# Performance work log

Measured on AMD Instinct MI355X. Metric: run time of the kernel, lower is better.

Reference implementation:

```python
import jax, jax.numpy as jnp
import numpy as np

SUB_NO = 20
T_NO = 200
T_DATA = 200000
E_NO = 400
I_NO = 100
N_BASIS = 20
COS_SHIFT = 1.0
COS_SCALE = 5.0


def make_cos_basis():
    # (N_BASIS, T_NO) raised-cosine basis in log time
    i = jnp.arange(N_BASIS, dtype=jnp.float32)[:, None]
    phi = (jnp.pi / 2.0) * i
    x = jnp.arange(T_NO, dtype=jnp.float32)[None, :]
    raw = COS_SCALE * jnp.log(x + COS_SHIFT)
    basis = 0.5 * jnp.cos(raw - phi) + 0.5
    keep = (raw >= phi - jnp.pi) & (raw <= phi + jnp.pi)
    return jnp.where(keep, basis, 0.0)


def grouped_causal_conv(syn, kern_flipped):
    # syn: (T, sub), kern_flipped: (sub, T_NO) already time-reversed -> causal filter
    x = jnp.pad(syn.T, ((0, 0), (T_NO - 1, 0)))[None]          # (1, sub, T+T_NO-1)
    out = jax.lax.conv_general_dilated(
        x, kern_flipped[:, None, :], (1,), 'VALID',
        dimension_numbers=('NCH', 'OIH', 'NCH'),
        feature_group_count=syn.shape[1])
    return out[0].T                                             # (T, sub)


def causal_conv1(z_pad, kern_flipped):
    # z_pad: (L,), kern_flipped: (T_NO,) -> valid conv, length L - T_NO + 1
    out = jax.lax.conv_general_dilated(
        z_pad[None, None, :], kern_flipped[None, None, :], (1,), 'VALID',
        dimension_numbers=('NCH', 'OIH', 'NCH'))
    return out[0, 0]


def setup_inputs() -> dict:
    key = jax.random.key(0)
    ks = jax.random.split(key, 12)
    S_e = (jax.random.uniform(ks[0], (T_DATA, E_NO)) < 0.05).astype(jnp.float32)
    S_i = (jax.random.uniform(ks[1], (T_DATA, I_NO)) < 0.05).astype(jnp.float32)
    Z = (jax.random.uniform(ks[2], (T_DATA,)) < 0.02).astype(jnp.float32)
    # binary-tree dendrite adjacency
    C_den = np.zeros((SUB_NO, SUB_NO), dtype=np.int32)
    for c in range(1, SUB_NO):
        C_den[(c - 1) // 2, c] = 1
    C_den = jnp.asarray(C_den)
    e_asn = np.asarray(jax.random.randint(ks[3], (E_NO,), 0, SUB_NO))
    i_asn = np.asarray(jax.random.randint(ks[4], (I_NO,), 0, SUB_NO))
    C_syn_e = np.zeros((SUB_NO, E_NO), dtype=np.float32); C_syn_e[e_asn, np.arange(E_NO)] = 1.0
    C_syn_i = np.zeros((SUB_NO, I_NO), dtype=np.float32); C_syn_i[i_asn, np.arange(I_NO)] = 1.0
    W_syn_ns = jax.random.uniform(ks[5], (SUB_NO, 2)) * 0.1
    W_syn_ns = W_syn_ns.at[:, 1].multiply(-1.0)
    return {
        'S_e': S_e, 'S_i': S_i, 'Z': Z,
        'C_den': C_den,
        'C_syn_e': jnp.asarray(C_syn_e), 'C_syn_i': jnp.asarray(C_syn_i),
        'W_syn_ns': W_syn_ns,
        'Tau_syn_ns': jnp.ones((SUB_NO, 2)) * 3.0,
        'Delta_syn_ns': jnp.zeros((SUB_NO, 2)),
        'W_syn_s': jax.random.normal(ks[6], (SUB_NO, N_BASIS, 2)) * 0.01,
        'W_sub_ns': jnp.ones(SUB_NO) * 0.1,
        'W_sub_s': jnp.ones(SUB_NO) * 0.1,
        'V_o': jax.random.normal(ks[7], (1,)),
        'Theta_ns': jnp.zeros(SUB_NO),
        'Theta_s': jnp.zeros(SUB_NO),
        'hist_s_weights': jax.random.normal(ks[8], (N_BASIS,)) * 0.01,
        'hist_ns_weights': jax.random.normal(ks[9], (N_BASIS,)) * 0.01,
    }


def reference(S_e, S_i, Z, C_den, C_syn_e, C_syn_i, W_syn_ns, Tau_syn_ns,
              Delta_syn_ns, W_syn_s, W_sub_ns, W_sub_s, V_o, Theta_ns,
              Theta_s, hist_s_weights, hist_ns_weights):
    cos_basis = make_cos_basis()
    # --- spike_convolve ---
    syn_e = S_e @ C_syn_e.T                                     # (T, sub)
    syn_i = S_i @ C_syn_i.T
    t = jnp.arange(T_NO, dtype=jnp.float32)[None, :]
    tau_e = Tau_syn_ns[:, 0:1] ** 2
    tau_i = Tau_syn_ns[:, 1:2] ** 2
    t_e = jnp.maximum(t - Delta_syn_ns[:, 0:1], 0.0) / tau_e
    t_i = jnp.maximum(t - Delta_syn_ns[:, 1:2], 0.0) / tau_i
    e_kern_ns = t_e * jnp.exp(-t_e) * W_syn_ns[:, 0:1] ** 2      # (sub, T_NO)
    i_kern_ns = -t_i * jnp.exp(-t_i) * W_syn_ns[:, 1:2] ** 2
    e_kern_s = (W_syn_s[:, :, 0] ** 2) @ cos_basis               # (sub, T_NO)
    i_kern_s = -(W_syn_s[:, :, 1] ** 2) @ cos_basis
    filt_e_ns = grouped_causal_conv(syn_e, jnp.flip(e_kern_ns, 1))
    filt_i_ns = grouped_causal_conv(syn_i, jnp.flip(i_kern_ns, 1))
    filt_e_s = grouped_causal_conv(syn_e, jnp.flip(e_kern_s, 1))
    filt_i_s = grouped_causal_conv(syn_i, jnp.flip(i_kern_s, 1))
    syn_ns = filt_e_ns + filt_i_ns
    syn_s = filt_e_s + filt_i_s
    # --- spike-history filtering of observed root spikes Z ---
    hist_s_kern = hist_s_weights @ cos_basis                     # (T_NO,)
    hist_ns_kern = hist_ns_weights @ cos_basis
    Z_pad = jnp.pad(Z, (T_NO, 0))                                # (T + T_NO,)
    hist_ns_filt = causal_conv1(Z_pad, jnp.flip(hist_ns_kern))[:-1]  # (T,)
    hist_s_filt = causal_conv1(Z_pad, jnp.flip(hist_s_kern))[:-1]
    # --- leaf-to-root tree recursion (unrolled over SUB_NO static nodes) ---
    C_den_f = C_den.astype(syn_s.dtype)
    w_s2 = W_sub_s ** 2
    w_ns2 = W_sub_ns ** 2
    T_data = S_e.shape[0]
    s_out = jnp.zeros((T_data, SUB_NO), dtype=syn_s.dtype)
    ns_out = jnp.zeros((T_data, SUB_NO), dtype=syn_ns.dtype)
    for idx in range(SUB_NO - 1, 0, -1):
        child_s = s_out @ (C_den_f[idx] * w_s2)                  # (T,) 0 if leaf
        child_ns = ns_out @ (C_den_f[idx] * w_ns2)
        s_out = s_out.at[:, idx].set(jnp.tanh(syn_s[:, idx] + child_s + Theta_s[idx]))
        ns_out = ns_out.at[:, idx].set(jnp.tanh(syn_ns[:, idx] + child_ns + Theta_ns[idx]))
    root_child_s = s_out @ (C_den_f[0] * w_s2)
    root_child_ns = ns_out @ (C_den_f[0] * w_ns2)
    s0 = jax.nn.sigmoid(hist_s_filt + syn_s[:, 0] + root_child_s + Theta_s[0])
    ns0 = jnp.tanh(hist_ns_filt + syn_ns[:, 0] + root_child_ns + Theta_ns[0])
    final_V = ns0 * w_ns2[0] + V_o
    final_Z = s0
    out_filters = jnp.vstack((e_kern_ns, i_kern_ns, e_kern_s, i_kern_s,
                              hist_ns_kern[None, :], hist_s_kern[None, :]))
    return final_V, final_Z, out_filters
```

## Files before the change

### kernel.cpp

```cpp
#include <hip/hip_runtime.h>

#define T_DATA 200000
#define E_NO 400
#define I_NO 100
#define SUB_NO 20
#define N_BASIS 20
#define T_NO 200

typedef unsigned short u16;
typedef unsigned int u32;
typedef unsigned long long u64;

#define WS_K4    0
#define WS_HIST2 64000
#define WS_MASKS 65600
#define WS_SYNE  131072
#define WS_SYNI  (WS_SYNE + 8000000)
#define WS_SNS   (WS_SYNI + 8000000)
#define WS_SS    (WS_SNS + 8000000)
#define WS_HF    (WS_SS + 8000000)

__device__ __forceinline__ u16 f2bf(float f) {
    union { float f; u32 u; } v; v.f = f;
    u32 u = v.u;
    u32 lsb = (u >> 16) & 1u;
    u += 0x7fffu + lsb;
    return (u16)(u >> 16);
}
__device__ __forceinline__ float bf2f(u16 b) {
    union { u32 u; float f; } v; v.u = ((u32)b) << 16; return v.f;
}
__device__ __forceinline__ void unpack8(uint4 u, float* x) {
    union { u32 u; float f; } c;
    c.u = u.x << 16;          x[0] = c.f;
    c.u = u.x & 0xffff0000u;  x[1] = c.f;
    c.u = u.y << 16;          x[2] = c.f;
    c.u = u.y & 0xffff0000u;  x[3] = c.f;
    c.u = u.z << 16;          x[4] = c.f;
    c.u = u.z & 0xffff0000u;  x[5] = c.f;
    c.u = u.w << 16;          x[6] = c.f;
    c.u = u.w & 0xffff0000u;  x[7] = c.f;
}
__device__ __forceinline__ float fast_tanh(float x) {
    x = fminf(fmaxf(x, -15.f), 15.f);
    float e = __expf(2.f * x);
    return 1.f - 2.f / (e + 1.f);
}
__device__ __forceinline__ float fast_sigmoid(float x) {
    x = fminf(fmaxf(x, -30.f), 30.f);
    return 1.f / (1.f + __expf(-x));
}

__global__ __launch_bounds__(256) void k_setup(
    const float* __restrict__ Wns, const float* __restrict__ Tau,
    const float* __restrict__ Del, const float* __restrict__ Wsyns,
    const float* __restrict__ HwS, const float* __restrict__ HwNS,
    const float* __restrict__ Cse, const float* __restrict__ Csi,
    float4* __restrict__ k4, float2* __restrict__ hist2,
    u32* __restrict__ masks32, float* __restrict__ outF)
{
    __shared__ float cb[N_BASIS * T_NO];
    __shared__ u32 m32[480];
    const int tid = threadIdx.x;
    const int b = blockIdx.x;
    const float PI = 3.14159265358979323846f;

    if (b == 21) {
        for (int k = tid; k < 480; k += 256) m32[k] = 0;
        __syncthreads();
        for (int j = tid; j < E_NO; j += 256) {
            int a = 0;
            for (int s = 0; s < SUB_NO; ++s)
                if (Cse[s * E_NO + j] > 0.5f) a = s;
            int ch = j >> 8, r = j & 255, ln = r >> 2, cp = r & 3;
            int widx = (a * 8 + ch * 4 + cp) * 2 + (ln >> 5);
            atomicOr(&m32[widx], 1u << (ln & 31));
        }
        for (int j = tid; j < I_NO; j += 256) {
            int a = 0;
            for (int s = 0; s < SUB_NO; ++s)
                if (Csi[s * I_NO + j] > 0.5f) a = s;
            int ln = j >> 2, cp = j & 3;
            int widx = 320 + (a * 4 + cp) * 2 + (ln >> 5);
            atomicOr(&m32[widx], 1u << (ln & 31));
        }
        __syncthreads();
        for (int k = tid; k < 480; k += 256) masks32[k] = m32[k];
        return;
    }

    for (int it = tid; it < N_BASIS * T_NO; it += 256) {
        int bb = it / T_NO, j = it - bb * T_NO;
        float phi = 1.57079632679489662f * (float)bb;
        float raw = 5.0f * logf((float)j + 1.0f);
        float v = 0.f;
        if (raw >= phi - PI && raw <= phi + PI) v = 0.5f * cosf(raw - phi) + 0.5f;
        cb[it] = v;
    }
    __syncthreads();

    if (b < 20) {
        const int s = b;
        if (tid < T_NO) {
            const int j = tid;
            float tau_e = Tau[s * 2 + 0]; tau_e *= tau_e;
            float tau_i = Tau[s * 2 + 1]; tau_i *= tau_i;
            float de = Del[s * 2 + 0], di = Del[s * 2 + 1];
            float we = Wns[s * 2 + 0]; we *= we;
            float wi = Wns[s * 2 + 1]; wi *= wi;
            float te = fmaxf((float)j - de, 0.f) / tau_e;
            float ti = fmaxf((float)j - di, 0.f) / tau_i;
            float eNs = te * expf(-te) * we;
            float iNs = -ti * expf(-ti) * wi;
            float eS = 0.f, iS = 0.f;
            for (int bb = 0; bb < N_BASIS; ++bb) {
                float w0 = Wsyns[(s * N_BASIS + bb) * 2 + 0];
                float w1 = Wsyns[(s * N_BASIS + bb) * 2 + 1];
                float c = cb[bb * T_NO + j];
                eS += w0 * w0 * c;
                iS -= w1 * w1 * c;
            }
            int it = s * T_NO + j;
            k4[it] = make_float4(eNs, iNs, eS, iS);
            outF[it]         = eNs;
            outF[4000 + it]  = iNs;
            outF[8000 + it]  = eS;
            outF[12000 + it] = iS;
        }
    } else {
        if (tid < T_NO) {
            const int j = tid;
            float hn = 0.f, hs = 0.f;
            for (int bb = 0; bb < N_BASIS; ++bb) {
                float c = cb[bb * T_NO + j];
                hn += HwNS[bb] * c;
                hs += HwS[bb] * c;
            }
            hist2[j] = make_float2(hn, hs);
            outF[16000 + j] = hn;
            outF[16200 + j] = hs;
        }
    }
}

__global__ __launch_bounds__(256) void k_spikes(
    const float* __restrict__ Se, const float* __restrict__ Si,
    const u64* __restrict__ masks,
    u16* __restrict__ synEb, u16* __restrict__ synIb)
{
    __shared__ u16 tile[4][40 * 66];
    const int tid = threadIdx.x;
    const int wv = tid >> 6, lane = tid & 63;
    const int t0 = (blockIdx.x * 4 + wv) * 64;
    if (t0 >= T_DATA) return;

    u64 me0 = 0, me1 = 0, me2 = 0, me3 = 0, me4 = 0, me5 = 0, me6 = 0, me7 = 0;
    u64 mi0 = 0, mi1 = 0, mi2 = 0, mi3 = 0;
    if (lane < 20) {
        const u64* mp = masks + lane * 8;
        me0 = mp[0]; me1 = mp[1]; me2 = mp[2]; me3 = mp[3];
        me4 = mp[4]; me5 = mp[5]; me6 = mp[6]; me7 = mp[7];
    } else if (lane < 40) {
        const u64* mp = masks + 160 + (lane - 20) * 4;
        mi0 = mp[0]; mi1 = mp[1]; mi2 = mp[2]; mi3 = mp[3];
    }
    u16* tw = tile[wv];

#pragma unroll 2
    for (int tt = 0; tt < 64; ++tt) {
        const int t = t0 + tt;
        const float4* rE = (const float4*)(Se + (size_t)t * E_NO);
        const float4* rI = (const float4*)(Si + (size_t)t * I_NO);
        float4 e0 = rE[lane];
        float4 e1 = make_float4(0.f, 0.f, 0.f, 0.f);
        if (lane < 36) e1 = rE[64 + lane];
        float4 i0 = make_float4(0.f, 0.f, 0.f, 0.f);
        if (lane < 25) i0 = rI[lane];
        u64 b0 = __ballot(e0.x != 0.f);
        u64 b1 = __ballot(e0.y != 0.f);
        u64 b2 = __ballot(e0.z != 0.f);
        u64 b3 = __ballot(e0.w != 0.f);
        u64 b4 = __ballot(e1.x != 0.f);
        u64 b5 = __ballot(e1.y != 0.f);
        u64 b6 = __ballot(e1.z != 0.f);
        u64 b7 = __ballot(e1.w != 0.f);
        u64 c0 = __ballot(i0.x != 0.f);
        u64 c1 = __ballot(i0.y != 0.f);
        u64 c2 = __ballot(i0.z != 0.f);
        u64 c3 = __ballot(i0.w != 0.f);
        if (lane < 20) {
            int c = __popcll(b0 & me0) + __popcll(b1 & me1)
                  + __popcll(b2 & me2) + __popcll(b3 & me3)
                  + __popcll(b4 & me4) + __popcll(b5 & me5)
                  + __popcll(b6 & me6) + __popcll(b7 & me7);
            tw[lane * 66 + tt] = (u16)c;
        } else if (lane < 40) {
            int c = __popcll(c0 & mi0) + __popcll(c1 & mi1)
                  + __popcll(c2 & mi2) + __popcll(c3 & mi3);
            tw[lane * 66 + tt] = (u16)c;
        }
    }
    asm volatile("s_waitcnt lgkmcnt(0)" ::: "memory");

#pragma unroll 4
    for (int s = 0; s < 40; ++s) {
        float f = (float)tw[s * 66 + lane];
        u16 b = f2bf(f);
        if (s < 20) synEb[(size_t)s * T_DATA + t0 + lane] = b;
        else        synIb[(size_t)(s - 20) * T_DATA + t0 + lane] = b;
    }
}

#define TT 512
#define WROW 712
__global__ __launch_bounds__(256) void k_conv(
    const u16* __restrict__ synEb, const u16* __restrict__ synIb,
    const float* __restrict__ Z,
    const float4* __restrict__ k4g, const float2* __restrict__ hist2g,
    u16* __restrict__ synNSb, u16* __restrict__ synSb,
    float2* __restrict__ hfilt)
{
    __shared__ __align__(16) u16 wE[4 * WROW];
    __shared__ __align__(16) u16 wI[4 * WROW];
    __shared__ __align__(16) float4 k4l[4 * T_NO];
    const int tid = threadIdx.x;
    const int t0 = blockIdx.x * TT;
    const int g  = blockIdx.y;
    const int W0 = t0 - 200;

    if (g < 5) {
        for (int q = tid; q < 712; q += 256) {
            int arr = (q >= 356) ? 1 : 0;
            int qq = q - arr * 356;
            int row = qq / 89, c = qq - row * 89;
            int s = g * 4 + row;
            const u16* src = (arr ? synIb : synEb) + (size_t)s * T_DATA;
            u16* dst = (arr ? wI : wE) + row * WROW + c * 8;
            int gg = W0 + c * 8;
            if (gg >= 0 && gg + 8 <= T_DATA) {
                *(uint4*)dst = *(const uint4*)(src + gg);
            } else {
                for (int e = 0; e < 8; ++e) {
                    int t = gg + e;
                    dst[e] = (t >= 0 && t < T_DATA) ? src[t] : (u16)0;
                }
            }
        }
        for (int q = tid; q < 800; q += 256) {
            int su = q / 200, j = q - su * 200;
            k4l[q] = k4g[(g * 4 + su) * T_NO + j];
        }
    } else {
        for (int q = tid; q < 623; q += 256) {
            if (q < 356) ((uint4*)wI)[q] = make_uint4(0, 0, 0, 0);
            else         ((uint4*)wE)[q - 356 + 89] = make_uint4(0, 0, 0, 0);
        }
        for (int c = tid; c < 89; c += 256) {
            int gg = W0 + c * 8;
            u16 zb[8];
            for (int e = 0; e < 8; ++e) {
                int t = gg + e;
                zb[e] = (t >= 0 && t < T_DATA) ? f2bf(Z[t]) : (u16)0;
            }
            u32 w0 = (u32)zb[0] | ((u32)zb[1] << 16);
            u32 w1 = (u32)zb[2] | ((u32)zb[3] << 16);
            u32 w2 = (u32)zb[4] | ((u32)zb[5] << 16);
            u32 w3 = (u32)zb[6] | ((u32)zb[7] << 16);
            *(uint4*)(wE + c * 8) = make_uint4(w0, w1, w2, w3);
        }
        for (int q = tid; q < 800; q += 256) {
            int su = q / 200, j = q - su * 200;
            float4 v = make_float4(0.f, 0.f, 0.f, 0.f);
            if (su == 0) {
                float2 h = hist2g[j];
                v = make_float4(h.x, 0.f, h.y, 0.f);
            }
            k4l[q] = v;
        }
    }
    __syncthreads();

    const int wv = tid >> 6;
    const int slot = tid & 63;
    const int bT = slot * 8;
    const u16* rowE = wE + wv * WROW;
    const u16* rowI = wI + wv * WROW;

    float aN[8], aS2[8];
#pragma unroll
    for (int m = 0; m < 8; ++m) { aN[m] = 0.f; aS2[m] = 0.f; }

#pragma unroll 1
    for (int jj = 0; jj <= 192; jj += 8) {
        const int p = bT + 192 - jj;
        float xe[16], xi[16];
        uint4 eA = *(const uint4*)(rowE + p);
        uint4 eB = *(const uint4*)(rowE + p + 8);
        uint4 iA = *(const uint4*)(rowI + p);
        uint4 iB = *(const uint4*)(rowI + p + 8);
        unpack8(eA, xe); unpack8(eB, xe + 8);
        unpack8(iA, xi); unpack8(iB, xi + 8);
#pragma unroll
        for (int k = 0; k < 8; ++k) {
            float4 kk = k4l[wv * T_NO + jj + k];
#pragma unroll
            for (int m = 0; m < 8; ++m) {
                float e = xe[m + 8 - k];
                float ii = xi[m + 8 - k];
                aN[m]  = fmaf(e, kk.x, fmaf(ii, kk.y, aN[m]));
                aS2[m] = fmaf(e, kk.z, fmaf(ii, kk.w, aS2[m]));
            }
        }
    }

    if (g < 5) {
        const int s = g * 4 + wv;
        const int t = t0 + bT;
        u32 w0 = (u32)f2bf(aN[0]) | ((u32)f2bf(aN[1]) << 16);
        u32 w1 = (u32)f2bf(aN[2]) | ((u32)f2bf(aN[3]) << 16);
        u32 w2 = (u32)f2bf(aN[4]) | ((u32)f2bf(aN[5]) << 16);
        u32 w3 = (u32)f2bf(aN[6]) | ((u32)f2bf(aN[7]) << 16);
        u32 v0 = (u32)f2bf(aS2[0]) | ((u32)f2bf(aS2[1]) << 16);
        u32 v1 = (u32)f2bf(aS2[2]) | ((u32)f2bf(aS2[3]) << 16);
        u32 v2 = (u32)f2bf(aS2[4]) | ((u32)f2bf(aS2[5]) << 16);
        u32 v3 = (u32)f2bf(aS2[6]) | ((u32)f2bf(aS2[7]) << 16);
        if (t + 8 <= T_DATA) {
            *(uint4*)(synNSb + (size_t)s * T_DATA + t) = make_uint4(w0, w1, w2, w3);
            *(uint4*)(synSb  + (size_t)s * T_DATA + t) = make_uint4(v0, v1, v2, v3);
        } else if (t < T_DATA) {
            for (int m = 0; m < 8 && t + m < T_DATA; ++m) {
                synNSb[(size_t)s * T_DATA + t + m] = f2bf(aN[m]);
                synSb[(size_t)s * T_DATA + t + m] = f2bf(aS2[m]);
            }
        }
    } else if (wv == 0) {
#pragma unroll
        for (int m = 0; m < 8; ++m) {
            int tt = t0 + bT + m + 1;
            if (tt < T_DATA) hfilt[tt] = make_float2(aN[m], aS2[m]);
        }
        if (blockIdx.x == 0 && tid == 0) hfilt[0] = make_float2(0.f, 0.f);
    }
}

#define CT 256
__global__ __launch_bounds__(256) void k_tree(
    const u16* __restrict__ synNSb, const u16* __restrict__ synSb,
    const float2* __restrict__ hfilt,
    const int* __restrict__ Cden,
    const float* __restrict__ WsubNS, const float* __restrict__ WsubS,
    const float* __restrict__ Vo, const float* __restrict__ ThNS,
    const float* __restrict__ ThS,
    float* __restrict__ outV, float* __restrict__ outZ)
{
    __shared__ __align__(16) u16 lNS[SUB_NO * CT];
    __shared__ __align__(16) u16 lS[SUB_NO * CT];
    __shared__ float AS[SUB_NO][SUB_NO], AN[SUB_NO][SUB_NO];
    __shared__ float ths[SUB_NO], thn[SUB_NO];
    __shared__ float wn20s, vos;
    const int tid = threadIdx.x;
    const int t0 = blockIdx.x * CT;

    for (int q = tid; q < 1280; q += 256) {
        int arr = (q >= 640) ? 1 : 0;
        int qq = q - arr * 640;
        int row = qq >> 5, c = qq & 31;
        const u16* src = (arr ? synSb : synNSb) + (size_t)row * T_DATA;
        u16* dst = (arr ? lS : lNS) + row * CT + c * 8;
        int gg = t0 + c * 8;
        if (gg + 8 <= T_DATA) {
            *(uint4*)dst = *(const uint4*)(src + gg);
        } else {
            for (int e = 0; e < 8; ++e) {
                int t = gg + e;
                dst[e] = (t < T_DATA) ? src[t] : (u16)0;
            }
        }
    }
    for (int k = tid; k < SUB_NO * SUB_NO; k += 256) {
        int idx = k / SUB_NO, c = k - idx * SUB_NO;
        float m = (float)Cden[k];
        float wsv = WsubS[c];
        float wnv = WsubNS[c];
        AS[idx][c] = m * wsv * wsv;
        AN[idx][c] = m * wnv * wnv;
    }
    if (tid < SUB_NO) { ths[tid] = ThS[tid]; thn[tid] = ThNS[tid]; }
    if (tid == 0) {
        float w = WsubNS[0];
        wn20s = w * w;
        vos = Vo[0];
    }
    __syncthreads();

    const int t = t0 + tid;
    float2 hf = make_float2(0.f, 0.f);
    if (t < T_DATA) hf = hfilt[t];

    float vs[SUB_NO], vn[SUB_NO];
#pragma unroll
    for (int c = 0; c < SUB_NO; ++c) { vs[c] = 0.f; vn[c] = 0.f; }
#pragma unroll
    for (int idx = SUB_NO - 1; idx >= 1; --idx) {
        float cs = 0.f, cn = 0.f;
#pragma unroll
        for (int c = 0; c < SUB_NO; ++c) {
            cs = fmaf(AS[idx][c], vs[c], cs);
            cn = fmaf(AN[idx][c], vn[c], cn);
        }
        float synS_v = bf2f(lS[idx * CT + tid]);
        float synN_v = bf2f(lNS[idx * CT + tid]);
        vs[idx] = fast_tanh(synS_v + cs + ths[idx]);
        vn[idx] = fast_tanh(synN_v + cn + thn[idx]);
    }
    float cs0 = 0.f, cn0 = 0.f;
#pragma unroll
    for (int c = 0; c < SUB_NO; ++c) {
        cs0 = fmaf(AS[0][c], vs[c], cs0);
        cn0 = fmaf(AN[0][c], vn[c], cn0);
    }
    float s0  = fast_sigmoid(hf.y + bf2f(lS[tid]) + cs0 + ths[0]);
    float ns0 = fast_tanh(hf.x + bf2f(lNS[tid]) + cn0 + thn[0]);

    if (t < T_DATA) {
        outV[t] = ns0 * wn20s + vos;
        outZ[t] = s0;
    }
}

extern "C" void kernel_launch(void* const* d_in, const int* in_sizes, int n_in,
                              void* d_out, int out_size, void* d_ws, size_t ws_size,
                              hipStream_t stream)
{
    const float* Se    = (const float*)d_in[0];
    const float* Si    = (const float*)d_in[1];
    const float* Z     = (const float*)d_in[2];
    const int*   Cden  = (const int*)d_in[3];
    const float* Cse   = (const float*)d_in[4];
    const float* Csi   = (const float*)d_in[5];
    const float* Wns   = (const float*)d_in[6];
    const float* Tau   = (const float*)d_in[7];
    const float* Del   = (const float*)d_in[8];
    const float* Wsyns = (const float*)d_in[9];
    const float* WsubNS= (const float*)d_in[10];
    const float* WsubS = (const float*)d_in[11];
    const float* Vo    = (const float*)d_in[12];
    const float* ThNS  = (const float*)d_in[13];
    const float* ThS   = (const float*)d_in[14];
    const float* HwS   = (const float*)d_in[15];
    const float* HwNS  = (const float*)d_in[16];

    char* ws = (char*)d_ws;
    float4* k4    = (float4*)(ws + WS_K4);
    float2* hist2 = (float2*)(ws + WS_HIST2);
    u64*    masks = (u64*)(ws + WS_MASKS);
    u16*    synEb = (u16*)(ws + WS_SYNE);
    u16*    synIb = (u16*)(ws + WS_SYNI);
    u16*    synNSb= (u16*)(ws + WS_SNS);
    u16*    synSb = (u16*)(ws + WS_SS);
    float2* hfilt = (float2*)(ws + WS_HF);

    float* outV = (float*)d_out;
    float* outZ = outV + T_DATA;
    float* outF = outV + 2 * T_DATA;

    k_setup<<<22, 256, 0, stream>>>(Wns, Tau, Del, Wsyns, HwS, HwNS, Cse, Csi,
                                    k4, hist2, (u32*)masks, outF);
    k_spikes<<<(3125 + 3) / 4, 256, 0, stream>>>(Se, Si, masks, synEb, synIb);
    dim3 gc((T_DATA + TT - 1) / TT, 6);
    k_conv<<<gc, 256, 0, stream>>>(synEb, synIb, Z, k4, hist2,
                                   synNSb, synSb, hfilt);
    k_tree<<<(T_DATA + CT - 1) / CT, 256, 0, stream>>>(
        synNSb, synSb, hfilt, Cden, WsubNS, WsubS, Vo, ThNS, ThS,
        outV, outZ);
}
```

Baseline: 634.1 us.

## Switch convolution to packed fp16 dot2 with interleaved E/I streams and sliding register window

Stores spike counts and filter taps as packed fp16 pairs (excitatory and inhibitory interleaved), so the causal convolution runs on v_dot2 instructions, each handling both input streams per tap. Taps are pre-reversed and read straight from global memory (wave-uniform) instead of being staged in LDS, and inputs slide through a register window. k_spikes is split into more, smaller blocks that write the interleaved layout. Intermediates move from bf16 to fp16, which adds range and rounding risk for larger accumulated values.

After: 606.1 us (median of 2 runs). -4.4%, faster.

```diff
diff --git a/kernel.cpp b/kernel.cpp
--- a/kernel.cpp
+++ b/kernel.cpp
@@ -10,36 +10,27 @@
 typedef unsigned short u16;
 typedef unsigned int u32;
 typedef unsigned long long u64;
-
-#define WS_K4    0
-#define WS_HIST2 64000
-#define WS_MASKS 65600
-#define WS_SYNE  131072
-#define WS_SYNI  (WS_SYNE + 8000000)
-#define WS_SNS   (WS_SYNI + 8000000)
+typedef _Float16 hf;
+typedef _Float16 half2_t __attribute__((ext_vector_type(2)));
+
+#define WS_KT    0
+#define WS_MASKS 33600
+#define WS_SYNEI 65536
+#define WS_SNS   (WS_SYNEI + 16000000)
 #define WS_SS    (WS_SNS + 8000000)
 #define WS_HF    (WS_SS + 8000000)
 
-__device__ __forceinline__ u16 f2bf(float f) {
-    union { float f; u32 u; } v; v.f = f;
-    u32 u = v.u;
-    u32 lsb = (u >> 16) & 1u;
-    u += 0x7fffu + lsb;
-    return (u16)(u >> 16);
-}
-__device__ __forceinline__ float bf2f(u16 b) {
-    union { u32 u; float f; } v; v.u = ((u32)b) << 16; return v.f;
-}
-__device__ __forceinline__ void unpack8(uint4 u, float* x) {
-    union { u32 u; float f; } c;
-    c.u = u.x << 16;          x[0] = c.f;
-    c.u = u.x & 0xffff0000u;  x[1] = c.f;
-    c.u = u.y << 16;          x[2] = c.f;
-    c.u = u.y & 0xffff0000u;  x[3] = c.f;
-    c.u = u.z << 16;          x[4] = c.f;
-    c.u = u.z & 0xffff0000u;  x[5] = c.f;
-    c.u = u.w << 16;          x[6] = c.f;
-    c.u = u.w & 0xffff0000u;  x[7] = c.f;
+__device__ __forceinline__ u16 f2h(float f) {
+    hf h = (hf)f; u16 b; __builtin_memcpy(&b, &h, 2); return b;
+}
+__device__ __forceinline__ float h2f(u16 b) {
+    hf h; __builtin_memcpy(&h, &b, 2); return (float)h;
+}
+__device__ __forceinline__ float dot2(u32 a, u32 b, float c) {
+    half2_t ha, hb;
+    __builtin_memcpy(&ha, &a, 4);
+    __builtin_memcpy(&hb, &b, 4);
+    return __builtin_amdgcn_fdot2(ha, hb, c, false);
 }
 __device__ __forceinline__ float fast_tanh(float x) {
     x = fminf(fmaxf(x, -15.f), 15.f);
@@ -56,8 +47,8 @@
     const float* __restrict__ Del, const float* __restrict__ Wsyns,
     const float* __restrict__ HwS, const float* __restrict__ HwNS,
     const float* __restrict__ Cse, const float* __restrict__ Csi,
-    float4* __restrict__ k4, float2* __restrict__ hist2,
-    u32* __restrict__ masks32, float* __restrict__ outF)
+    uint2* __restrict__ ktap, u32* __restrict__ masks32,
+    float* __restrict__ outF)
 {
     __shared__ float cb[N_BASIS * T_NO];
     __shared__ u32 m32[480];
@@ -121,11 +112,13 @@
                 iS -= w1 * w1 * c;
             }
             int it = s * T_NO + j;
-            k4[it] = make_float4(eNs, iNs, eS, iS);
             outF[it]         = eNs;
             outF[4000 + it]  = iNs;
             outF[8000 + it]  = eS;
             outF[12000 + it] = iS;
+            u32 pN = (u32)f2h(eNs) | ((u32)f2h(iNs) << 16);
+            u32 pS = (u32)f2h(eS)  | ((u32)f2h(iS)  << 16);
+            ktap[s * T_NO + (199 - j)] = make_uint2(pN, pS);
         }
     } else {
         if (tid < T_NO) {
@@ -136,9 +129,9 @@
                 hn += HwNS[bb] * c;
                 hs += HwS[bb] * c;
             }
-            hist2[j] = make_float2(hn, hs);
             outF[16000 + j] = hn;
             outF[16200 + j] = hs;
+            ktap[20 * T_NO + (199 - j)] = make_uint2((u32)f2h(hn), (u32)f2h(hs));
         }
     }
 }
@@ -146,13 +139,12 @@
 __global__ __launch_bounds__(256) void k_spikes(
     const float* __restrict__ Se, const float* __restrict__ Si,
     const u64* __restrict__ masks,
-    u16* __restrict__ synEb, u16* __restrict__ synIb)
+    u32* __restrict__ synEI)
 {
-    __shared__ u16 tile[4][40 * 66];
+    __shared__ u16 tile[4][40 * 18];
     const int tid = threadIdx.x;
     const int wv = tid >> 6, lane = tid & 63;
-    const int t0 = (blockIdx.x * 4 + wv) * 64;
-    if (t0 >= T_DATA) return;
+    const int t0 = (blockIdx.x * 4 + wv) * 16;
 
     u64 me0 = 0, me1 = 0, me2 = 0, me3 = 0, me4 = 0, me5 = 0, me6 = 0, me7 = 0;
     u64 mi0 = 0, mi1 = 0, mi2 = 0, mi3 = 0;
@@ -167,7 +159,7 @@
     u16* tw = tile[wv];
 
 #pragma unroll 2
-    for (int tt = 0; tt < 64; ++tt) {
+    for (int tt = 0; tt < 16; ++tt) {
         const int t = t0 + tt;
         const float4* rE = (const float4*)(Se + (size_t)t * E_NO);
         const float4* rI = (const float4*)(Si + (size_t)t * I_NO);
@@ -193,89 +185,70 @@
                   + __popcll(b2 & me2) + __popcll(b3 & me3)
                   + __popcll(b4 & me4) + __popcll(b5 & me5)
                   + __popcll(b6 & me6) + __popcll(b7 & me7);
-            tw[lane * 66 + tt] = (u16)c;
+            tw[lane * 18 + tt] = (u16)c;
         } else if (lane < 40) {
             int c = __popcll(c0 & mi0) + __popcll(c1 & mi1)
                   + __popcll(c2 & mi2) + __popcll(c3 & mi3);
-            tw[lane * 66 + tt] = (u16)c;
+            tw[lane * 18 + tt] = (u16)c;
         }
     }
     asm volatile("s_waitcnt lgkmcnt(0)" ::: "memory");
 
-#pragma unroll 4
-    for (int s = 0; s < 40; ++s) {
-        float f = (float)tw[s * 66 + lane];
-        u16 b = f2bf(f);
-        if (s < 20) synEb[(size_t)s * T_DATA + t0 + lane] = b;
-        else        synIb[(size_t)(s - 20) * T_DATA + t0 + lane] = b;
+    if (lane < 16) {
+#pragma unroll
+        for (int s = 0; s < 20; ++s) {
+            float fe = (float)tw[s * 18 + lane];
+            float fi = (float)tw[(20 + s) * 18 + lane];
+            u32 v = (u32)f2h(fe) | ((u32)f2h(fi) << 16);
+            synEI[(size_t)s * T_DATA + t0 + lane] = v;
+        }
     }
 }
 
 #define TT 512
 #define WROW 712
 __global__ __launch_bounds__(256) void k_conv(
-    const u16* __restrict__ synEb, const u16* __restrict__ synIb,
-    const float* __restrict__ Z,
-    const float4* __restrict__ k4g, const float2* __restrict__ hist2g,
+    const u32* __restrict__ synEI, const float* __restrict__ Z,
+    const uint2* __restrict__ ktap,
     u16* __restrict__ synNSb, u16* __restrict__ synSb,
     float2* __restrict__ hfilt)
 {
-    __shared__ __align__(16) u16 wE[4 * WROW];
-    __shared__ __align__(16) u16 wI[4 * WROW];
-    __shared__ __align__(16) float4 k4l[4 * T_NO];
+    __shared__ __align__(16) u32 wEI[4 * WROW];
     const int tid = threadIdx.x;
     const int t0 = blockIdx.x * TT;
     const int g  = blockIdx.y;
     const int W0 = t0 - 200;
 
     if (g < 5) {
-        for (int q = tid; q < 712; q += 256) {
-            int arr = (q >= 356) ? 1 : 0;
-            int qq = q - arr * 356;
-            int row = qq / 89, c = qq - row * 89;
+        for (int q = tid; q < 4 * 178; q += 256) {
+            int row = q / 178, c = q - row * 178;
             int s = g * 4 + row;
-            const u16* src = (arr ? synIb : synEb) + (size_t)s * T_DATA;
-            u16* dst = (arr ? wI : wE) + row * WROW + c * 8;
-            int gg = W0 + c * 8;
-            if (gg >= 0 && gg + 8 <= T_DATA) {
+            const u32* src = synEI + (size_t)s * T_DATA;
+            u32* dst = wEI + row * WROW + c * 4;
+            int gg = W0 + c * 4;
+            if (gg >= 0 && gg + 4 <= T_DATA) {
                 *(uint4*)dst = *(const uint4*)(src + gg);
             } else {
-                for (int e = 0; e < 8; ++e) {
+#pragma unroll
+                for (int e = 0; e < 4; ++e) {
                     int t = gg + e;
-                    dst[e] = (t >= 0 && t < T_DATA) ? src[t] : (u16)0;
+                    dst[e] = (t >= 0 && t < T_DATA) ? src[t] : 0u;
                 }
             }
         }
-        for (int q = tid; q < 800; q += 256) {
-            int su = q / 200, j = q - su * 200;
-            k4l[q] = k4g[(g * 4 + su) * T_NO + j];
-        }
     } else {
-        for (int q = tid; q < 623; q += 256) {
-            if (q < 356) ((uint4*)wI)[q] = make_uint4(0, 0, 0, 0);
-            else         ((uint4*)wE)[q - 356 + 89] = make_uint4(0, 0, 0, 0);
-        }
-        for (int c = tid; c < 89; c += 256) {
-            int gg = W0 + c * 8;
-            u16 zb[8];
-            for (int e = 0; e < 8; ++e) {
+        for (int q = tid; q < 3 * 178; q += 256)
+            ((uint4*)(wEI + WROW))[q] = make_uint4(0, 0, 0, 0);
+        for (int c = tid; c < 178; c += 256) {
+            int gg = W0 + c * 4;
+            u32 o[4];
+#pragma unroll
+            for (int e = 0; e < 4; ++e) {
                 int t = gg + e;
-                zb[e] = (t >= 0 && t < T_DATA) ? f2bf(Z[t]) : (u16)0;
-            }
-            u32 w0 = (u32)zb[0] | ((u32)zb[1] << 16);
-            u32 w1 = (u32)zb[2] | ((u32)zb[3] << 16);
-            u32 w2 = (u32)zb[4] | ((u32)zb[5] << 16);
-            u32 w3 = (u32)zb[6] | ((u32)zb[7] << 16);
-            *(uint4*)(wE + c * 8) = make_uint4(w0, w1, w2, w3);
-        }
-        for (int q = tid; q < 800; q += 256) {
-            int su = q / 200, j = q - su * 200;
-            float4 v = make_float4(0.f, 0.f, 0.f, 0.f);
-            if (su == 0) {
-                float2 h = hist2g[j];
-                v = make_float4(h.x, 0.f, h.y, 0.f);
-            }
-            k4l[q] = v;
+                float z = (t >= 0 && t < T_DATA) ? Z[t] : 0.f;
+                o[e] = (u32)f2h(z);
+            }
+            *(uint4*)(wEI + c * 4) = make_uint4(o[0], o[1], o[2], o[3]);
         }
     }
     __syncthreads();
@@ -283,61 +256,74 @@
     const int wv = tid >> 6;
     const int slot = tid & 63;
     const int bT = slot * 8;
-    const u16* rowE = wE + wv * WROW;
-    const u16* rowI = wI + wv * WROW;
-
-    float aN[8], aS2[8];
-#pragma unroll
-    for (int m = 0; m < 8; ++m) { aN[m] = 0.f; aS2[m] = 0.f; }
+    const u32* row = wEI + wv * WROW;
+    const int su = (g < 5) ? (g * 4 + wv) : 20;
+    const uint2* kt = ktap + (size_t)__builtin_amdgcn_readfirstlane(su) * T_NO;
+
+    float aN[8], aS[8];
+#pragma unroll
+    for (int m = 0; m < 8; ++m) { aN[m] = 0.f; aS[m] = 0.f; }
+
+    u32 x[16];
+    {
+        uint4 wA = *(const uint4*)(row + bT);
+        uint4 wB = *(const uint4*)(row + bT + 4);
+        uint4 wC = *(const uint4*)(row + bT + 8);
+        uint4 wD = *(const uint4*)(row + bT + 12);
+        x[0]=wA.x; x[1]=wA.y; x[2]=wA.z; x[3]=wA.w;
+        x[4]=wB.x; x[5]=wB.y; x[6]=wB.z; x[7]=wB.w;
+        x[8]=wC.x; x[9]=wC.y; x[10]=wC.z; x[11]=wC.w;
+        x[12]=wD.x; x[13]=wD.y; x[14]=wD.z; x[15]=wD.w;
+    }
 
 #pragma unroll 1
     for (int jj = 0; jj <= 192; jj += 8) {
-        const int p = bT + 192 - jj;
-        float xe[16], xi[16];
-        uint4 eA = *(const uint4*)(rowE + p);
-        uint4 eB = *(const uint4*)(rowE + p + 8);
-        uint4 iA = *(const uint4*)(rowI + p);
-        uint4 iB = *(const uint4*)(rowI + p + 8);
-        unpack8(eA, xe); unpack8(eB, xe + 8);
-        unpack8(iA, xi); unpack8(iB, xi + 8);
+        uint2 kp[8];
+#pragma unroll
+        for (int k = 0; k < 8; ++k) kp[k] = kt[jj + k];
 #pragma unroll
         for (int k = 0; k < 8; ++k) {
-            float4 kk = k4l[wv * T_NO + jj + k];
 #pragma unroll
             for (int m = 0; m < 8; ++m) {
-                float e = xe[m + 8 - k];
-                float ii = xi[m + 8 - k];
-                aN[m]  = fmaf(e, kk.x, fmaf(ii, kk.y, aN[m]));
-                aS2[m] = fmaf(e, kk.z, fmaf(ii, kk.w, aS2[m]));
-            }
+                aN[m] = dot2(x[m + 1 + k], kp[k].x, aN[m]);
+                aS[m] = dot2(x[m + 1 + k], kp[k].y, aS[m]);
+            }
+        }
+        if (jj < 192) {
+#pragma unroll
+            for (int i = 0; i < 8; ++i) x[i] = x[i + 8];
+            uint4 nA = *(const uint4*)(row + bT + jj + 16);
+            uint4 nB = *(const uint4*)(row + bT + jj + 20);
+            x[8]=nA.x; x[9]=nA.y; x[10]=nA.z; x[11]=nA.w;
+            x[12]=nB.x; x[13]=nB.y; x[14]=nB.z; x[15]=nB.w;
         }
     }
 
     if (g < 5) {
         const int s = g * 4 + wv;
         const int t = t0 + bT;
-        u32 w0 = (u32)f2bf(aN[0]) | ((u32)f2bf(aN[1]) << 16);
-        u32 w1 = (u32)f2bf(aN[2]) | ((u32)f2bf(aN[3]) << 16);
-        u32 w2 = (u32)f2bf(aN[4]) | ((u32)f2bf(aN[5]) << 16);
-        u32 w3 = (u32)f2bf(aN[6]) | ((u32)f2bf(aN[7]) << 16);
-        u32 v0 = (u32)f2bf(aS2[0]) | ((u32)f2bf(aS2[1]) << 16);
-        u32 v1 = (u32)f2bf(aS2[2]) | ((u32)f2bf(aS2[3]) << 16);
-        u32 v2 = (u32)f2bf(aS2[4]) | ((u32)f2bf(aS2[5]) << 16);
-        u32 v3 = (u32)f2bf(aS2[6]) | ((u32)f2bf(aS2[7]) << 16);
+        u32 w0 = (u32)f2h(aN[0]) | ((u32)f2h(aN[1]) << 16);
+        u32 w1 = (u32)f2h(aN[2]) | ((u32)f2h(aN[3]) << 16);
+        u32 w2 = (u32)f2h(aN[4]) | ((u32)f2h(aN[5]) << 16);
+        u32 w3 = (u32)f2h(aN[6]) | ((u32)f2h(aN[7]) << 16);
+        u32 v0 = (u32)f2h(aS[0]) | ((u32)f2h(aS[1]) << 16);
+        u32 v1 = (u32)f2h(aS[2]) | ((u32)f2h(aS[3]) << 16);
+        u32 v2 = (u32)f2h(aS[4]) | ((u32)f2h(aS[5]) << 16);
+        u32 v3 = (u32)f2h(aS[6]) | ((u32)f2h(aS[7]) << 16);
         if (t + 8 <= T_DATA) {
             *(uint4*)(synNSb + (size_t)s * T_DATA + t) = make_uint4(w0, w1, w2, w3);
             *(uint4*)(synSb  + (size_t)s * T_DATA + t) = make_uint4(v0, v1, v2, v3);
         } else if (t < T_DATA) {
             for (int m = 0; m < 8 && t + m < T_DATA; ++m) {
-                synNSb[(size_t)s * T_DATA + t + m] = f2bf(aN[m]);
-                synSb[(size_t)s * T_DATA + t + m] = f2bf(aS2[m]);
+                synNSb[(size_t)s * T_DATA + t + m] = f2h(aN[m]);
+                synSb[(size_t)s * T_DATA + t + m] = f2h(aS[m]);
             }
         }
     } else if (wv == 0) {
 #pragma unroll
         for (int m = 0; m < 8; ++m) {
             int tt = t0 + bT + m + 1;
-            if (tt < T_DATA) hfilt[tt] = make_float2(aN[m], aS2[m]);
+            if (tt < T_DATA) hfilt[tt] = make_float2(aN[m], aS[m]);
         }
         if (blockIdx.x == 0 && tid == 0) hfilt[0] = make_float2(0.f, 0.f);
     }
@@ -408,8 +394,8 @@
             cs = fmaf(AS[idx][c], vs[c], cs);
             cn = fmaf(AN[idx][c], vn[c], cn);
         }
-        float synS_v = bf2f(lS[idx * CT + tid]);
-        float synN_v = bf2f(lNS[idx * CT + tid]);
+        float synS_v = h2f(lS[idx * CT + tid]);
+        float synN_v = h2f(lNS[idx * CT + tid]);
         vs[idx] = fast_tanh(synS_v + cs + ths[idx]);
         vn[idx] = fast_tanh(synN_v + cn + thn[idx]);
     }
@@ -419,8 +405,8 @@
         cs0 = fmaf(AS[0][c], vs[c], cs0);
         cn0 = fmaf(AN[0][c], vn[c], cn0);
     }
-    float s0  = fast_sigmoid(hf.y + bf2f(lS[tid]) + cs0 + ths[0]);
-    float ns0 = fast_tanh(hf.x + bf2f(lNS[tid]) + cn0 + thn[0]);
+    float s0  = fast_sigmoid(hf.y + h2f(lS[tid]) + cs0 + ths[0]);
+    float ns0 = fast_tanh(hf.x + h2f(lNS[tid]) + cn0 + thn[0]);
 
     if (t < T_DATA) {
         outV[t] = ns0 * wn20s + vos;
@@ -451,11 +437,9 @@
     const float* HwNS  = (const float*)d_in[16];
 
     char* ws = (char*)d_ws;
-    float4* k4    = (float4*)(ws + WS_K4);
-    float2* hist2 = (float2*)(ws + WS_HIST2);
+    uint2*  ktap  = (uint2*)(ws + WS_KT);
     u64*    masks = (u64*)(ws + WS_MASKS);
-    u16*    synEb = (u16*)(ws + WS_SYNE);
-    u16*    synIb = (u16*)(ws + WS_SYNI);
+    u32*    synEI = (u32*)(ws + WS_SYNEI);
     u16*    synNSb= (u16*)(ws + WS_SNS);
     u16*    synSb = (u16*)(ws + WS_SS);
     float2* hfilt = (float2*)(ws + WS_HF);
@@ -465,11 +449,10 @@
     float* outF = outV + 2 * T_DATA;
 
     k_setup<<<22, 256, 0, stream>>>(Wns, Tau, Del, Wsyns, HwS, HwNS, Cse, Csi,
-                                    k4, hist2, (u32*)masks, outF);
-    k_spikes<<<(3125 + 3) / 4, 256, 0, stream>>>(Se, Si, masks, synEb, synIb);
+                                    ktap, (u32*)masks, outF);
+    k_spikes<<<3125, 256, 0, stream>>>(Se, Si, masks, synEI);
     dim3 gc((T_DATA + TT - 1) / TT, 6);
-    k_conv<<<gc, 256, 0, stream>>>(synEb, synIb, Z, k4, hist2,
-                                   synNSb, synSb, hfilt);
+    k_conv<<<gc, 256, 0, stream>>>(synEI, Z, ktap, synNSb, synSb, hfilt);
     k_tree<<<(T_DATA + CT - 1) / CT, 256, 0, stream>>>(
         synNSb, synSb, hfilt, Cden, WsubNS, WsubS, Vo, ThNS, ThS,
         outV, outZ);
```
